# Kernel optimization log

Measured on AMD Instinct MI355X. Metric: run time of the kernel, lower is better.

## Reference

```python
import jax, jax.numpy as jnp
import numpy as np

B = 8; N_MELS = 128; T_LEN = 1024; PH = 16; PW = 16
D = 768          # embed_dim
DEPTH = 12
N = 16           # d_state
K = 4            # d_conv (mamba default)
E = 2 * D        # d_inner (expand=2)
R = 48           # dt_rank = ceil(D/16)
NC = 10
LP = (N_MELS // PH) * (T_LEN // PW)   # 512 patch tokens
MID = LP // 2                          # middle cls token position


def layer_norm(x, w, b, eps=1e-5):
    m = x.mean(-1, keepdims=True)
    v = ((x - m) ** 2).mean(-1, keepdims=True)
    return (x - m) * jax.lax.rsqrt(v + eps) * w + b


def dw_conv(x, w, b):
    # x: (B,L,E), w: (E,K) -> causal depthwise conv1d + SiLU (mamba conv branch)
    xt = jnp.transpose(x, (0, 2, 1))
    y = jax.lax.conv_general_dilated(xt, w[:, None, :], (1,), [(K - 1, 0)],
                                     feature_group_count=E,
                                     dimension_numbers=('NCH', 'OIH', 'NCH'))
    return jax.nn.silu(jnp.transpose(y + b[None, :, None], (0, 2, 1)))


def ssm(u, z, xw, dtw, dtb, A_log, Dp):
    # selective scan: u,z (B,L,E); xw (R+2N,E); dtw (E,R); A_log,Dp (E,N)/(E,)
    dbc = jnp.einsum('ble,re->blr', u, xw)
    dt, Bm, Cm = dbc[..., :R], dbc[..., R:R + N], dbc[..., R + N:]
    delta = jax.nn.softplus(jnp.einsum('blr,er->ble', dt, dtw) + dtb)
    A = -jnp.exp(A_log)  # (E,N)

    def step(h, inp):
        d_t, B_t, C_t, u_t = inp  # (B,E),(B,N),(B,N),(B,E)
        h = h * jnp.exp(d_t[:, :, None] * A) + (d_t * u_t)[:, :, None] * B_t[:, None, :]
        return h, jnp.einsum('ben,bn->be', h, C_t)

    h0 = jnp.zeros((u.shape[0], E, N), u.dtype)
    xs = (jnp.transpose(delta, (1, 0, 2)), jnp.transpose(Bm, (1, 0, 2)),
          jnp.transpose(Cm, (1, 0, 2)), jnp.transpose(u, (1, 0, 2)))
    _, ys = jax.lax.scan(step, h0, xs)
    y = jnp.transpose(ys, (1, 0, 2)) + u * Dp
    return y * jax.nn.silu(z)


def setup_inputs() -> dict:
    key = jax.random.key(0)
    kit = iter(jax.random.split(key, 64))
    def nrm(shape, s=0.02):
        return jax.random.normal(next(kit), shape, jnp.float32) * s
    inp = {}
    inp['x'] = jax.random.normal(next(kit), (B, 1, N_MELS, T_LEN), jnp.float32)
    inp['patch_w'] = nrm((D, 1, PH, PW))
    inp['patch_b'] = jnp.zeros((D,), jnp.float32)
    inp['cls_token'] = nrm((1, 1, D))
    inp['norm_w'] = jnp.ones((DEPTH, D), jnp.float32)
    inp['norm_b'] = jnp.zeros((DEPTH, D), jnp.float32)
    inp['in_proj_w'] = nrm((DEPTH, 2 * E, D))
    for s in ('f', 'b'):
        inp['conv_w_' + s] = nrm((DEPTH, E, K), 0.1)
        inp['conv_b_' + s] = jnp.zeros((DEPTH, E), jnp.float32)
        inp['x_proj_w_' + s] = nrm((DEPTH, R + 2 * N, E))
        inp['dt_proj_w_' + s] = nrm((DEPTH, E, R), 0.1)
        dt = jnp.exp(jax.random.uniform(next(kit), (DEPTH, E), jnp.float32)
                     * (np.log(0.1) - np.log(1e-3)) + np.log(1e-3))
        inp['dt_proj_b_' + s] = jnp.log(jnp.expm1(dt))  # inverse softplus init
        inp['A_log_' + s] = jnp.broadcast_to(
            jnp.log(jnp.arange(1, N + 1, dtype=jnp.float32)), (DEPTH, E, N)) + jnp.zeros((DEPTH, E, N), jnp.float32)
        inp['D_' + s] = jnp.ones((DEPTH, E), jnp.float32)
    inp['out_proj_w'] = nrm((DEPTH, D, E))
    inp['fnorm_w'] = jnp.ones((D,), jnp.float32)
    inp['fnorm_b'] = jnp.zeros((D,), jnp.float32)
    inp['head_norm_w'] = jnp.ones((D,), jnp.float32)
    inp['head_norm_b'] = jnp.zeros((D,), jnp.float32)
    inp['head_w'] = nrm((NC, D))
    inp['head_b'] = jnp.zeros((NC,), jnp.float32)
    return inp


def reference(x, patch_w, patch_b, cls_token, norm_w, norm_b, in_proj_w,
              conv_w_f, conv_b_f, conv_w_b, conv_b_b,
              x_proj_w_f, x_proj_w_b, dt_proj_w_f, dt_proj_b_f,
              dt_proj_w_b, dt_proj_b_b, A_log_f, A_log_b, D_f, D_b,
              out_proj_w, fnorm_w, fnorm_b, head_norm_w, head_norm_b,
              head_w, head_b):
    # patch embed (Conv2d, stride = patch)
    t = jax.lax.conv_general_dilated(x, patch_w, (PH, PW), 'VALID',
                                     dimension_numbers=('NCHW', 'OIHW', 'NCHW'))
    t = t + patch_b[None, :, None, None]
    b = t.shape[0]
    tok = jnp.transpose(t.reshape(b, D, -1), (0, 2, 1))  # (B, LP, D)
    cls = jnp.broadcast_to(cls_token, (b, 1, D))
    h = jnp.concatenate([tok[:, :MID], cls, tok[:, MID:]], axis=1)  # middle cls token
    for i in range(DEPTH):
        hn = layer_norm(h, norm_w[i], norm_b[i])
        xz = jnp.einsum('bld,ed->ble', hn, in_proj_w[i])
        xm, z = xz[..., :E], xz[..., E:]
        # forward direction
        xf = dw_conv(xm, conv_w_f[i], conv_b_f[i])
        yf = ssm(xf, z, x_proj_w_f[i], dt_proj_w_f[i], dt_proj_b_f[i], A_log_f[i], D_f[i])
        # backward direction (bimamba v2): scan over flipped sequence
        xr, zr = xm[:, ::-1], z[:, ::-1]
        xb = dw_conv(xr, conv_w_b[i], conv_b_b[i])
        yb = ssm(xb, zr, x_proj_w_b[i], dt_proj_w_b[i], dt_proj_b_b[i], A_log_b[i], D_b[i])[:, ::-1]
        h = h + jnp.einsum('ble,de->bld', yf + yb, out_proj_w[i])
    h = layer_norm(h, fnorm_w, fnorm_b)
    feat = h[:, MID]  # middle cls token feature
    feat = layer_norm(feat, head_norm_w, head_norm_b)
    return jnp.einsum('bd,cd->bc', feat, head_w) + head_b
```

## Files before the change

### kernel.cpp

```cpp
#include <hip/hip_runtime.h>
#include <cstddef>
#include <cstdint>

#define NB     8
#define L_SEQ  513
#define DMODEL 768
#define EDIM   1536
#define XZDIM  3072
#define NSTATE 16
#define DBCW   80
#define RDIM   48
#define ROWS   (NB*L_SEQ)
#define RE     ((size_t)ROWS*EDIM)
#define KSPLIT_DBC 8

typedef unsigned short u16;
typedef __bf16 bf16x8 __attribute__((ext_vector_type(8)));
typedef float  f32x4  __attribute__((ext_vector_type(4)));

__device__ __forceinline__ u16 f2b(float f) {
  uint32_t x = __float_as_uint(f);
  uint32_t r = x + 0x7fffu + ((x >> 16) & 1u);
  return (u16)(r >> 16);
}

__device__ __forceinline__ void glds16(const void* g, void* l) {
  __builtin_amdgcn_global_load_lds(
      (const __attribute__((address_space(1))) uint32_t*)g,
      (__attribute__((address_space(3))) uint32_t*)l, 16, 0, 0);
}

__global__ __launch_bounds__(256) void f2b_k(const float* __restrict__ in,
                                             u16* __restrict__ out, int n)
{
  int i = (blockIdx.x*256 + threadIdx.x) * 4;
  if (i >= n) return;
  float4 v = *reinterpret_cast<const float4*>(in + i);
  ushort4 o;
  o.x = f2b(v.x); o.y = f2b(v.y); o.z = f2b(v.z); o.w = f2b(v.w);
  *reinterpret_cast<ushort4*>(out + i) = o;
}

__global__ __launch_bounds__(256) void f2b2_k(const float* __restrict__ a,
                                              const float* __restrict__ b,
                                              u16* __restrict__ oa,
                                              u16* __restrict__ ob,
                                              int n1, int n2)
{
  int i = (blockIdx.x*256 + threadIdx.x) * 4;
  if (i < n1) {
    float4 v = *reinterpret_cast<const float4*>(a + i);
    ushort4 o; o.x=f2b(v.x); o.y=f2b(v.y); o.z=f2b(v.z); o.w=f2b(v.w);
    *reinterpret_cast<ushort4*>(oa + i) = o;
  } else {
    int j = i - n1;
    if (j < n2) {
      float4 v = *reinterpret_cast<const float4*>(b + j);
      ushort4 o; o.x=f2b(v.x); o.y=f2b(v.y); o.z=f2b(v.z); o.w=f2b(v.w);
      *reinterpret_cast<ushort4*>(ob + j) = o;
    }
  }
}

__global__ __launch_bounds__(256) void cvt_dtw_k(const float* __restrict__ in,
                                                 u16* __restrict__ out, int nrows)
{
  int idx = blockIdx.x*256 + threadIdx.x;
  if (idx >= nrows*16) return;
  int row = idx >> 4, c4 = (idx & 15) * 4;
  ushort4 o; o.x = o.y = o.z = o.w = 0;
  if (c4 < RDIM) {
    float4 v = *reinterpret_cast<const float4*>(in + (size_t)row*RDIM + c4);
    o.x = f2b(v.x); o.y = f2b(v.y); o.z = f2b(v.z); o.w = f2b(v.w);
  }
  *reinterpret_cast<ushort4*>(out + (size_t)row*64 + c4) = o;
}

__global__ __launch_bounds__(256) void im2col_k(const float* __restrict__ x,
                                                u16* __restrict__ P)
{
  int idx = blockIdx.x*256 + threadIdx.x;
  int col4 = (idx & 63) * 4;
  int r = idx >> 6;
  int b = r >> 9, p = r & 511;
  int ph = p >> 6, pcol = p & 63;
  int i = col4 >> 4, j = col4 & 15;
  const float* src = x + (size_t)b*131072 + (size_t)(ph*16 + i)*1024 + pcol*16 + j;
  float4 v = *reinterpret_cast<const float4*>(src);
  ushort4 o;
  o.x = f2b(v.x); o.y = f2b(v.y); o.z = f2b(v.z); o.w = f2b(v.w);
  *reinterpret_cast<ushort4*>(P + (size_t)r*256 + col4) = o;
}

__global__ __launch_bounds__(256) void insert_k(const float* __restrict__ tokf,
                                                const float* __restrict__ cls,
                                                float* __restrict__ h)
{
  int idx = blockIdx.x*256 + threadIdx.x;
  if (idx >= ROWS*192) return;
  int d4 = (idx % 192) * 4;
  int row = idx / 192;
  int b = row / L_SEQ, l = row - b*L_SEQ;
  float4 v;
  if (l == 256) v = *reinterpret_cast<const float4*>(cls + d4);
  else {
    int p = (l < 256) ? l : l - 1;
    v = *reinterpret_cast<const float4*>(tokf + ((size_t)(b*512 + p))*DMODEL + d4);
  }
  *reinterpret_cast<float4*>(h + (size_t)row*DMODEL + d4) = v;
}

__device__ __forceinline__ void wave_reduce2(float& s, float& ss) {
  #pragma unroll
  for (int o = 32; o; o >>= 1) { s += __shfl_down(s, o); ss += __shfl_down(ss, o); }
}

__global__ __launch_bounds__(256) void layernorm_k(
    const float* __restrict__ x, const float* __restrict__ w,
    const float* __restrict__ b, u16* __restrict__ y)
{
  int row = blockIdx.x;
  const float* xr = x + (size_t)row*DMODEL;
  u16*         yr = y + (size_t)row*DMODEL;
  int t = threadIdx.x;
  float v0 = xr[t], v1 = xr[t+256], v2 = xr[t+512];
  float s = v0+v1+v2, ss = v0*v0 + v1*v1 + v2*v2;
  wave_reduce2(s, ss);
  __shared__ float sm[8];
  if ((t & 63) == 0) { sm[t>>6] = s; sm[4 + (t>>6)] = ss; }
  __syncthreads();
  s  = sm[0]+sm[1]+sm[2]+sm[3];
  ss = sm[4]+sm[5]+sm[6]+sm[7];
  float mean = s * (1.f/768.f);
  float var  = ss * (1.f/768.f) - mean*mean;
  float rstd = rsqrtf(var + 1e-5f);
  yr[t]     = f2b((v0-mean)*rstd*w[t]     + b[t]);
  yr[t+256] = f2b((v1-mean)*rstd*w[t+256] + b[t+256]);
  yr[t+512] = f2b((v2-mean)*rstd*w[t+512] + b[t+512]);
}

__global__ __launch_bounds__(256) void gemm_bf16_k(
    const u16* __restrict__ A, int lda,
    const u16* __restrict__ W, int ldw,
    float* __restrict__ C, int ldc, int M, int Ncols, int K,
    const float* __restrict__ bias, int epilogue,
    int zsplit, size_t bsA, size_t bsW, size_t bsC, size_t bsBias)
{
  __shared__ __align__(16) u16 Asl[2][4096];
  __shared__ __align__(16) u16 Wsl[2][4096];
  const int tid = threadIdx.x;
  const int bm = blockIdx.y << 7, bn = blockIdx.x << 7;
  const int wv = tid >> 6, ln = tid & 63;
  const int wr = (wv >> 1) << 6, wc = (wv & 1) << 6;

  int kb = 0, ke = K;
  {
    int zb = (int)blockIdx.z;
    int dir = zb / zsplit, kslab = zb - dir*zsplit;
    A += (size_t)dir * bsA;
    W += (size_t)dir * bsW;
    C += (size_t)dir * bsC;
    if (bias) bias += (size_t)dir * bsBias;
    if (zsplit > 1) {
      int ksl = K / zsplit;
      kb = kslab * ksl; ke = kb + ksl;
      C += (size_t)kslab * (size_t)M * (size_t)ldc;
    }
  }

  const int q0 = (ln >> 4) * 8;
  const int r0 = wv*16 + (ln & 15);
  const int r1 = (wv+4)*16 + (ln & 15);

  int ar0 = bm + r0; if (ar0 >= M) ar0 = M-1;
  int ar1 = bm + r1; if (ar1 >= M) ar1 = M-1;
  int nr0 = bn + r0; if (nr0 >= Ncols) nr0 = Ncols-1;
  int nr1 = bn + r1; if (nr1 >= Ncols) nr1 = Ncols-1;
  const u16* A0 = A + (size_t)ar0*lda + q0;
  const u16* A1 = A + (size_t)ar1*lda + q0;
  const u16* W0 = W + (size_t)nr0*ldw + q0;
  const u16* W1 = W + (size_t)nr1*ldw + q0;

  auto STAGE = [&](int buf, int k0) {
    char* ab = (char*)&Asl[buf][0];
    char* wb = (char*)&Wsl[buf][0];
    glds16(A0 + k0, ab + wv*1024);
    glds16(A1 + k0, ab + 4096 + wv*1024);
    glds16(W0 + k0, wb + wv*1024);
    glds16(W1 + k0, wb + 4096 + wv*1024);
  };

  f32x4 acc[4][4];
  #pragma unroll
  for (int m = 0; m < 4; ++m)
    #pragma unroll
    for (int n = 0; n < 4; ++n) acc[m][n] = (f32x4){0.f,0.f,0.f,0.f};

  const int niter = (ke - kb) >> 5;
  STAGE(0, kb);
  for (int it = 0; it < niter; ++it) {
    const int p = it & 1;
    if (it + 1 < niter) {
      STAGE(p ^ 1, kb + (it + 1) * 32);
      asm volatile("s_waitcnt vmcnt(4)" ::: "memory");
    } else {
      asm volatile("s_waitcnt vmcnt(0)" ::: "memory");
    }
    __builtin_amdgcn_s_barrier();
    bf16x8 fa[4], fb[4];
    #pragma unroll
    for (int m = 0; m < 4; ++m)
      fa[m] = *reinterpret_cast<const bf16x8*>(&Asl[p][((wr>>4)+m)*512 + ln*8]);
    #pragma unroll
    for (int n = 0; n < 4; ++n)
      fb[n] = *reinterpret_cast<const bf16x8*>(&Wsl[p][((wc>>4)+n)*512 + ln*8]);
    #pragma unroll
    for (int m = 0; m < 4; ++m)
      #pragma unroll
      for (int n = 0; n < 4; ++n)
        acc[m][n] = __builtin_amdgcn_mfma_f32_16x16x32_bf16(fa[m], fb[n], acc[m][n], 0, 0, 0);
    __builtin_amdgcn_s_barrier();
  }

  const int crow0 = bm + wr + ((ln >> 4) << 2);
  const int ccol0 = bn + wc + (ln & 15);
  #pragma unroll
  for (int m = 0; m < 4; ++m) {
    #pragma unroll
    for (int q = 0; q < 4; ++q) {
      int row = crow0 + m*16 + q;
      if (row >= M) continue;
      float* Cr = C + (size_t)row*ldc;
      #pragma unroll
      for (int n = 0; n < 4; ++n) {
        int col = ccol0 + n*16;
        if (col >= Ncols) continue;
        float v = acc[m][n][q];
        if (epilogue == 1) v += Cr[col];
        else if (epilogue == 2) {
          v += bias[col];
          v = fmaxf(v, 0.f) + log1pf(__expf(-fabsf(v)));
        } else if (epilogue == 3) v += bias[col];
        Cr[col] = v;
      }
    }
  }
}

__global__ void reduce_split2_k(const float* __restrict__ part,
                                float* __restrict__ dbc2, u16* __restrict__ dt48,
                                int nsplit)
{
  int i = blockIdx.x * 256 + threadIdx.x;
  if (i >= 2*ROWS*DBCW) return;
  int dir = i / (ROWS*DBCW);
  int j   = i - dir*(ROWS*DBCW);
  const float* p = part + (size_t)dir*nsplit*(ROWS*DBCW);
  float s = 0.f;
  for (int z = 0; z < nsplit; ++z) s += p[(size_t)z*(ROWS*DBCW) + j];
  dbc2[i] = s;
  int row = j / DBCW, col = j - row*DBCW;
  if (col < RDIM)    dt48[(size_t)dir*ROWS*64 + (size_t)row*64 + col] = f2b(s);
  else if (col < 64) dt48[(size_t)dir*ROWS*64 + (size_t)row*64 + col] = 0;
}

__global__ __launch_bounds__(256) void dwconv_silu_k(
    const float* __restrict__ xz,
    const float* __restrict__ w_f, const float* __restrict__ w_b,
    const float* __restrict__ b_f, const float* __restrict__ b_b,
    u16* __restrict__ outb2)
{
  const int dir = blockIdx.y;
  const float* w    = dir ? w_b : w_f;
  const float* bias = dir ? b_b : b_f;
  u16* outb = outb2 + (size_t)dir*RE;
  int idx = blockIdx.x * 256 + threadIdx.x;
  int r = idx / (EDIM/4);
  int e4 = (idx - r*(EDIM/4)) * 4;
  int b = r / L_SEQ, t = r - b*L_SEQ;
  float4 acc = *reinterpret_cast<const float4*>(&bias[e4]);
  float4 wq0 = *reinterpret_cast<const float4*>(&w[(size_t)(e4+0)*4]);
  float4 wq1 = *reinterpret_cast<const float4*>(&w[(size_t)(e4+1)*4]);
  float4 wq2 = *reinterpret_cast<const float4*>(&w[(size_t)(e4+2)*4]);
  float4 wq3 = *reinterpret_cast<const float4*>(&w[(size_t)(e4+3)*4]);
  #pragma unroll
  for (int k = 0; k < 4; ++k) {
    int tt = t - 3 + k;
    if (tt >= 0) {
      int phys = dir ? (L_SEQ-1 - tt) : tt;
      float4 xv = *reinterpret_cast<const float4*>(
          &xz[((size_t)b*L_SEQ + phys)*XZDIM + e4]);
      float w0 = (k==0)?wq0.x:(k==1)?wq0.y:(k==2)?wq0.z:wq0.w;
      float w1 = (k==0)?wq1.x:(k==1)?wq1.y:(k==2)?wq1.z:wq1.w;
      float w2 = (k==0)?wq2.x:(k==1)?wq2.y:(k==2)?wq2.z:wq2.w;
      float w3 = (k==0)?wq3.x:(k==1)?wq3.y:(k==2)?wq3.z:wq3.w;
      acc.x = fmaf(xv.x, w0, acc.x);
      acc.y = fmaf(xv.y, w1, acc.y);
      acc.z = fmaf(xv.z, w2, acc.z);
      acc.w = fmaf(xv.w, w3, acc.w);
    }
  }
  float4 sv;
  sv.x = acc.x / (1.f + __expf(-acc.x));
  sv.y = acc.y / (1.f + __expf(-acc.y));
  sv.z = acc.z / (1.f + __expf(-acc.z));
  sv.w = acc.w / (1.f + __expf(-acc.w));
  ushort4 ob;
  ob.x = f2b(sv.x); ob.y = f2b(sv.y); ob.z = f2b(sv.z); ob.w = f2b(sv.w);
  *reinterpret_cast<ushort4*>(&outb[(size_t)r*EDIM + e4]) = ob;
}

__device__ __forceinline__ float dpp_reduce16(float v) {
  v += __int_as_float(__builtin_amdgcn_update_dpp(0, __float_as_int(v), 0x111, 0xf, 0xf, true));
  v += __int_as_float(__builtin_amdgcn_update_dpp(0, __float_as_int(v), 0x112, 0xf, 0xf, true));
  v += __int_as_float(__builtin_amdgcn_update_dpp(0, __float_as_int(v), 0x114, 0xf, 0xf, true));
  v += __int_as_float(__builtin_amdgcn_update_dpp(0, __float_as_int(v), 0x118, 0xf, 0xf, true));
  return v;
}

#define TC 32
#define NCH ((L_SEQ + TC - 1) / TC)

__global__ __launch_bounds__(256) void ssm_scan_k(
    const float* __restrict__ delta2, const u16* __restrict__ ub2,
    const float* __restrict__ dbc2,
    const float* __restrict__ Alf, const float* __restrict__ Alb,
    const float* __restrict__ Dpf, const float* __restrict__ Dpb,
    const float* __restrict__ xz,  u16* __restrict__ yhalf)
{
  __shared__ __align__(16) float dd[2][TC][16];
  __shared__ __align__(16) float us[2][TC][16];
  __shared__ __align__(16) float Bs[2][16][TC+4];
  __shared__ __align__(16) float Cs[2][16][TC+4];
  __shared__ __align__(16) float yb[TC][16];

  const int dir = blockIdx.z;
  const float* delta = delta2 + (size_t)dir*RE;
  const u16*   ub    = ub2    + (size_t)dir*RE;
  const float* dbc   = dbc2   + (size_t)dir*ROWS*DBCW;
  const float* A_log = dir ? Alb : Alf;
  const float* Dp    = dir ? Dpb : Dpf;
  u16* yh = yhalf + (size_t)dir*RE;

  const int tid = threadIdx.x;
  const int g = tid >> 4, n = tid & 15;
  const int b = blockIdx.y;
  const int e0 = blockIdx.x * 16;
  const int e = e0 + g;
  const size_t rb = (size_t)b * L_SEQ;

  const float a  = -__expf(A_log[(size_t)e*NSTATE + n]);
  const float dp = Dp[e];

  const int ss_ = tid >> 3;
  const int c2  = (tid & 7) * 2;
  const int j4  = (tid & 7) * 4;

  float2 dv = make_float2(0,0);
  uint32_t uv = 0;
  float4 bcv = make_float4(0,0,0,0);

  auto LOAD = [&](int c) {
    int Tn = min(TC, L_SEQ - c*TC);
    if (ss_ < Tn) {
      size_t r = rb + c*TC + ss_;
      dv  = *reinterpret_cast<const float2*>(&delta[r*EDIM + e0 + c2]);
      uv  = *reinterpret_cast<const uint32_t*>(&ub[r*EDIM + e0 + c2]);
      bcv = *reinterpret_cast<const float4*>(&dbc[r*DBCW + RDIM + j4]);
    }
  };
  auto STORE = [&](int p, int c) {
    int Tn = min(TC, L_SEQ - c*TC);
    if (ss_ < Tn) {
      dd[p][ss_][c2] = dv.x; dd[p][ss_][c2+1] = dv.y;
      us[p][ss_][c2]   = __uint_as_float((uv & 0xffffu) << 16);
      us[p][ss_][c2+1] = __uint_as_float(uv & 0xffff0000u);
      if (j4 < 16) {
        Bs[p][j4  ][ss_] = bcv.x; Bs[p][j4+1][ss_] = bcv.y;
        Bs[p][j4+2][ss_] = bcv.z; Bs[p][j4+3][ss_] = bcv.w;
      } else {
        Cs[p][j4-16][ss_] = bcv.x; Cs[p][j4-15][ss_] = bcv.y;
        Cs[p][j4-14][ss_] = bcv.z; Cs[p][j4-13][ss_] = bcv.w;
      }
    }
  };

  float hst = 0.f;
  LOAD(0);
  STORE(0, 0);
  __syncthreads();

  int p = 0;
  for (int c = 0; c < NCH; ++c) {
    const int t0 = c * TC;
    const int T  = min(TC, L_SEQ - t0);
    if (c + 1 < NCH) LOAD(c + 1);

    int s = 0;
    for (; s + 3 < T; s += 4) {
      float4 Bv = *reinterpret_cast<const float4*>(&Bs[p][n][s]);
      float4 Cv = *reinterpret_cast<const float4*>(&Cs[p][n][s]);
      #pragma unroll
      for (int i = 0; i < 4; ++i) {
        float Bt = (i==0)?Bv.x:(i==1)?Bv.y:(i==2)?Bv.z:Bv.w;
        float Ct = (i==0)?Cv.x:(i==1)?Cv.y:(i==2)?Cv.z:Cv.w;
        float d  = dd[p][s+i][g];
        float uu = us[p][s+i][g];
        hst = fmaf(hst, __expf(d*a), d*uu*Bt);
        float yp = dpp_reduce16(hst * Ct);
        if (n == 15) yb[s+i][g] = yp + uu*dp;
      }
    }
    for (; s < T; ++s) {
      float Bt = Bs[p][n][s], Ct = Cs[p][n][s];
      float d  = dd[p][s][g];
      float uu = us[p][s][g];
      hst = fmaf(hst, __expf(d*a), d*uu*Bt);
      float yp = dpp_reduce16(hst * Ct);
      if (n == 15) yb[s][g] = yp + uu*dp;
    }
    __syncthreads();

    if (ss_ < T) {
      int t = t0 + ss_;
      int phys = dir ? (L_SEQ-1 - t) : t;
      size_t pr = rb + phys;
      float2 yv = *reinterpret_cast<const float2*>(&yb[ss_][c2]);
      float2 zv = *reinterpret_cast<const float2*>(&xz[pr*XZDIM + EDIM + e0 + c2]);
      ushort2 o;
      o.x = f2b(yv.x * (zv.x / (1.f + __expf(-zv.x))));
      o.y = f2b(yv.y * (zv.y / (1.f + __expf(-zv.y))));
      *reinterpret_cast<ushort2*>(&yh[pr*EDIM + e0 + c2]) = o;
    }
    if (c + 1 < NCH) STORE(p ^ 1, c + 1);
    __syncthreads();
    p ^= 1;
  }
}

__global__ __launch_bounds__(256) void add_ybf_k(const u16* __restrict__ yhalf,
                                                 u16* __restrict__ ybf)
{
  size_t i = ((size_t)blockIdx.x*256 + threadIdx.x) * 8;
  uint4 a = *reinterpret_cast<const uint4*>(yhalf + i);
  uint4 b = *reinterpret_cast<const uint4*>(yhalf + RE + i);
  uint32_t av[4] = {a.x, a.y, a.z, a.w};
  uint32_t bv[4] = {b.x, b.y, b.z, b.w};
  uint32_t ov[4];
  #pragma unroll
  for (int q = 0; q < 4; ++q) {
    float lo = __uint_as_float((av[q] & 0xffffu) << 16) +
               __uint_as_float((bv[q] & 0xffffu) << 16);
    float hi = __uint_as_float(av[q] & 0xffff0000u) +
               __uint_as_float(bv[q] & 0xffff0000u);
    ov[q] = (uint32_t)f2b(lo) | ((uint32_t)f2b(hi) << 16);
  }
  uint4 o = {ov[0], ov[1], ov[2], ov[3]};
  *reinterpret_cast<uint4*>(ybf + i) = o;
}

__global__ __launch_bounds__(256) void head_k(
    const float* __restrict__ h,
    const float* __restrict__ fnw, const float* __restrict__ fnb,
    const float* __restrict__ hnw, const float* __restrict__ hnb,
    const float* __restrict__ hw,  const float* __restrict__ hb,
    float* __restrict__ out)
{
  int b = blockIdx.x, t = threadIdx.x;
  const float* xr = h + ((size_t)b*L_SEQ + 256)*DMODEL;
  __shared__ float feat[DMODEL];
  __shared__ float sm[8];
  float v0 = xr[t], v1 = xr[t+256], v2 = xr[t+512];
  float s = v0+v1+v2, ss = v0*v0+v1*v1+v2*v2;
  wave_reduce2(s, ss);
  if ((t & 63) == 0) { sm[t>>6] = s; sm[4+(t>>6)] = ss; }
  __syncthreads();
  s = sm[0]+sm[1]+sm[2]+sm[3]; ss = sm[4]+sm[5]+sm[6]+sm[7];
  float mean = s*(1.f/768.f), var = ss*(1.f/768.f) - mean*mean;
  float rstd = rsqrtf(var + 1e-5f);
  float f0 = (v0-mean)*rstd*fnw[t]     + fnb[t];
  float f1 = (v1-mean)*rstd*fnw[t+256] + fnb[t+256];
  float f2 = (v2-mean)*rstd*fnw[t+512] + fnb[t+512];
  s = f0+f1+f2; ss = f0*f0+f1*f1+f2*f2;
  wave_reduce2(s, ss);
  __syncthreads();
  if ((t & 63) == 0) { sm[t>>6] = s; sm[4+(t>>6)] = ss; }
  __syncthreads();
  s = sm[0]+sm[1]+sm[2]+sm[3]; ss = sm[4]+sm[5]+sm[6]+sm[7];
  mean = s*(1.f/768.f); var = ss*(1.f/768.f) - mean*mean;
  rstd = rsqrtf(var + 1e-5f);
  feat[t]     = (f0-mean)*rstd*hnw[t]     + hnb[t];
  feat[t+256] = (f1-mean)*rstd*hnw[t+256] + hnb[t+256];
  feat[t+512] = (f2-mean)*rstd*hnw[t+512] + hnb[t+512];
  __syncthreads();
  for (int c = 0; c < 10; ++c) {
    float d = 0.f;
    for (int i = t; i < DMODEL; i += 256) d = fmaf(feat[i], hw[(size_t)c*DMODEL + i], d);
    #pragma unroll
    for (int o = 32; o; o >>= 1) d += __shfl_down(d, o);
    __syncthreads();
    if ((t & 63) == 0) sm[t>>6] = d;
    __syncthreads();
    if (t == 0) out[b*10 + c] = sm[0]+sm[1]+sm[2]+sm[3] + hb[c];
  }
}

extern "C" void kernel_launch(void* const* d_in, const int* in_sizes, int n_in,
                              void* d_out, int out_size, void* d_ws, size_t ws_size,
                              hipStream_t stream)
{
  (void)in_sizes; (void)n_in; (void)out_size; (void)ws_size;
  const float* x           = (const float*)d_in[0];
  const float* patch_w     = (const float*)d_in[1];
  const float* patch_b     = (const float*)d_in[2];
  const float* cls_tok     = (const float*)d_in[3];
  const float* norm_w      = (const float*)d_in[4];
  const float* norm_b      = (const float*)d_in[5];
  const float* in_proj_w   = (const float*)d_in[6];
  const float* conv_w_f    = (const float*)d_in[7];
  const float* conv_b_f    = (const float*)d_in[8];
  const float* x_proj_w_f  = (const float*)d_in[9];
  const float* dt_proj_w_f = (const float*)d_in[10];
  const float* dt_proj_b_f = (const float*)d_in[11];
  const float* A_log_f     = (const float*)d_in[12];
  const float* D_f         = (const float*)d_in[13];
  const float* conv_w_b    = (const float*)d_in[14];
  const float* conv_b_b    = (const float*)d_in[15];
  const float* x_proj_w_b  = (const float*)d_in[16];
  const float* dt_proj_w_b = (const float*)d_in[17];
  const float* dt_proj_b_b = (const float*)d_in[18];
  const float* A_log_b     = (const float*)d_in[19];
  const float* D_b         = (const float*)d_in[20];
  const float* out_proj_w  = (const float*)d_in[21];
  const float* fnorm_w     = (const float*)d_in[22];
  const float* fnorm_b     = (const float*)d_in[23];
  const float* head_norm_w = (const float*)d_in[24];
  const float* head_norm_b = (const float*)d_in[25];
  const float* head_w      = (const float*)d_in[26];
  const float* head_b      = (const float*)d_in[27];
  float* out = (float*)d_out;

  float* ws = (float*)d_ws;
  float* h      = ws;        ws += (size_t)ROWS*DMODEL;
  u16*   hn     = (u16*)ws;  ws += RE/2;
  u16*   ybf    = hn;
  float* xz     = ws;        ws += (size_t)ROWS*XZDIM;
  u16*   ubufb2 = (u16*)ws;  ws += RE;
  float* dbc2   = ws;        ws += (size_t)2*ROWS*DBCW;
  u16*   dt48b2 = (u16*)ws;  ws += (size_t)2*ROWS*64/2;
  float* delta2 = ws;        ws += 2*RE;
  u16*   yhalf  = (u16*)ws;  ws += RE;
  u16*   wbf_a  = (u16*)ws;  ws += (size_t)XZDIM*DMODEL/2;
  u16*   wbf_b  = (u16*)ws;  ws += (size_t)DMODEL*EDIM/2;
  u16*   pwbf   = (u16*)ws;  ws += (size_t)DMODEL*256/2;
  u16*   xwbf   = (u16*)ws;  ws += (size_t)2*12*DBCW*EDIM/2;
  u16*   dtwbf  = (u16*)ws;  ws += (size_t)2*12*EDIM*64/2;
  float* dtb2   = ws;        ws += (size_t)2*12*EDIM;
  float* dbcp   = delta2;
  u16*   Pim    = ubufb2;
  float* tokf   = delta2;

  f2b_k<<<(DMODEL*256)/1024, 256, 0, stream>>>(patch_w, pwbf, DMODEL*256);
  f2b_k<<<(12*DBCW*EDIM)/1024, 256, 0, stream>>>(x_proj_w_f, xwbf, 12*DBCW*EDIM);
  f2b_k<<<(12*DBCW*EDIM)/1024, 256, 0, stream>>>(x_proj_w_b, xwbf + (size_t)12*DBCW*EDIM, 12*DBCW*EDIM);
  cvt_dtw_k<<<(12*EDIM*16)/256, 256, 0, stream>>>(dt_proj_w_f, dtwbf, 12*EDIM);
  cvt_dtw_k<<<(12*EDIM*16)/256, 256, 0, stream>>>(dt_proj_w_b, dtwbf + (size_t)12*EDIM*64, 12*EDIM);
  hipMemcpyAsync(dtb2,           dt_proj_b_f, (size_t)12*EDIM*4, hipMemcpyDeviceToDevice, stream);
  hipMemcpyAsync(dtb2 + 12*EDIM, dt_proj_b_b, (size_t)12*EDIM*4, hipMemcpyDeviceToDevice, stream);

  im2col_k<<<(4096*64)/256, 256, 0, stream>>>(x, Pim);
  {
    dim3 g(DMODEL/128, 4096/128);
    gemm_bf16_k<<<g, 256, 0, stream>>>(Pim, 256, pwbf, 256, tokf, DMODEL,
                                       4096, DMODEL, 256, patch_b, 3,
                                       1, 0, 0, 0, 0);
  }
  insert_k<<<(ROWS*192 + 255)/256, 256, 0, stream>>>(tokf, cls_tok, h);

  const int MT = (ROWS + 127)/128;

  for (int i = 0; i < 12; ++i) {
    f2b2_k<<<(XZDIM*DMODEL + DMODEL*EDIM)/1024, 256, 0, stream>>>(
        in_proj_w + (size_t)i*XZDIM*DMODEL, out_proj_w + (size_t)i*DMODEL*EDIM,
        wbf_a, wbf_b, XZDIM*DMODEL, DMODEL*EDIM);
    layernorm_k<<<ROWS, 256, 0, stream>>>(h, norm_w + (size_t)i*DMODEL,
                                          norm_b + (size_t)i*DMODEL, hn);
    {
      dim3 g(XZDIM/128, MT);
      gemm_bf16_k<<<g, 256, 0, stream>>>(hn, DMODEL, wbf_a, DMODEL,
                                         xz, XZDIM, ROWS, XZDIM, DMODEL, nullptr, 0,
                                         1, 0, 0, 0, 0);
    }
    {
      dim3 g((ROWS*EDIM/4)/256, 2);
      dwconv_silu_k<<<g, 256, 0, stream>>>(xz,
          conv_w_f + (size_t)i*EDIM*4, conv_w_b + (size_t)i*EDIM*4,
          conv_b_f + (size_t)i*EDIM,   conv_b_b + (size_t)i*EDIM, ubufb2);
    }
    {
      dim3 g(1, MT, 2*KSPLIT_DBC);
      gemm_bf16_k<<<g, 256, 0, stream>>>(ubufb2, EDIM,
          xwbf + (size_t)i*DBCW*EDIM, EDIM,
          dbcp, DBCW, ROWS, DBCW, EDIM, nullptr, 0,
          KSPLIT_DBC, RE, (size_t)12*DBCW*EDIM, (size_t)KSPLIT_DBC*ROWS*DBCW, 0);
      reduce_split2_k<<<(2*ROWS*DBCW + 255)/256, 256, 0, stream>>>(
          dbcp, dbc2, dt48b2, KSPLIT_DBC);
    }
    {
      dim3 g(EDIM/128, MT, 2);
      gemm_bf16_k<<<g, 256, 0, stream>>>(dt48b2, 64,
          dtwbf + (size_t)i*EDIM*64, 64,
          delta2, EDIM, ROWS, EDIM, 64, dtb2 + (size_t)i*EDIM, 2,
          1, (size_t)ROWS*64, (size_t)12*EDIM*64, RE, (size_t)12*EDIM);
    }
    {
      dim3 g(EDIM/16, NB, 2);
      ssm_scan_k<<<g, 256, 0, stream>>>(delta2, ubufb2, dbc2,
          A_log_f + (size_t)i*EDIM*NSTATE, A_log_b + (size_t)i*EDIM*NSTATE,
          D_f + (size_t)i*EDIM, D_b + (size_t)i*EDIM, xz, yhalf);
    }
    add_ybf_k<<<(int)(RE/8/256), 256, 0, stream>>>(yhalf, ybf);
    {
      dim3 g(DMODEL/128, MT);
      gemm_bf16_k<<<g, 256, 0, stream>>>(ybf, EDIM, wbf_b, EDIM,
                                         h, DMODEL, ROWS, DMODEL, EDIM, nullptr, 1,
                                         1, 0, 0, 0, 0);
    }
  }

  head_k<<<NB, 256, 0, stream>>>(h, fnorm_w, fnorm_b, head_norm_w, head_norm_b,
                                 head_w, head_b, out);
}
```

Baseline: 4.619 ms.

## Fuse bidirectional output sum into out-proj GEMM and narrow scan intermediates to bf16

The out_proj weight is duplicated along K, and the scan writes forward and backward outputs interleaved per row. The out-projection GEMM then runs with K=3072 and sums both directions itself, so the separate add kernel goes away. The in-proj GEMM now writes xm as fp32 and z as bf16 into separate buffers. Delta is stored in bf16 instead of fp32, and the scan's per-state reduction changes from a 16-lane DPP reduce to quad sums plus an LDS partial-sum buffer, with exp2f replacing expf. This cuts memory traffic and one launch in exchange for doubling the out-proj GEMM's K and lowering the precision of delta and z.

Result: slower. 5.299 ms (+14.7%).

```diff
diff --git a/kernel.cpp b/kernel.cpp
--- a/kernel.cpp
+++ b/kernel.cpp
@@ -23,6 +23,8 @@
   uint32_t r = x + 0x7fffu + ((x >> 16) & 1u);
   return (u16)(r >> 16);
 }
+__device__ __forceinline__ float b2flo(uint32_t w){ return __uint_as_float(w << 16); }
+__device__ __forceinline__ float b2fhi(uint32_t w){ return __uint_as_float(w & 0xffff0000u); }
 
 __device__ __forceinline__ void glds16(const void* g, void* l) {
   __builtin_amdgcn_global_load_lds(
@@ -57,7 +59,10 @@
     if (j < n2) {
       float4 v = *reinterpret_cast<const float4*>(b + j);
       ushort4 o; o.x=f2b(v.x); o.y=f2b(v.y); o.z=f2b(v.z); o.w=f2b(v.w);
-      *reinterpret_cast<ushort4*>(ob + j) = o;
+      int row = j / EDIM, col = j - row*EDIM;
+      u16* dst = ob + (size_t)row*XZDIM + col;
+      *reinterpret_cast<ushort4*>(dst)        = o;
+      *reinterpret_cast<ushort4*>(dst + EDIM) = o;
     }
   }
 }
@@ -142,7 +147,8 @@
 __global__ __launch_bounds__(256) void gemm_bf16_k(
     const u16* __restrict__ A, int lda,
     const u16* __restrict__ W, int ldw,
-    float* __restrict__ C, int ldc, int M, int Ncols, int K,
+    float* __restrict__ C, u16* __restrict__ Cb,
+    int ldc, int M, int Ncols, int K,
     const float* __restrict__ bias, int epilogue,
     int zsplit, size_t bsA, size_t bsW, size_t bsC, size_t bsBias)
 {
@@ -159,7 +165,8 @@
     int dir = zb / zsplit, kslab = zb - dir*zsplit;
     A += (size_t)dir * bsA;
     W += (size_t)dir * bsW;
-    C += (size_t)dir * bsC;
+    if (C)  C  += (size_t)dir * bsC;
+    if (Cb) Cb += (size_t)dir * bsC;
     if (bias) bias += (size_t)dir * bsBias;
     if (zsplit > 1) {
       int ksl = K / zsplit;
@@ -230,18 +237,25 @@
     for (int q = 0; q < 4; ++q) {
       int row = crow0 + m*16 + q;
       if (row >= M) continue;
-      float* Cr = C + (size_t)row*ldc;
       #pragma unroll
       for (int n = 0; n < 4; ++n) {
         int col = ccol0 + n*16;
         if (col >= Ncols) continue;
         float v = acc[m][n][q];
-        if (epilogue == 1) v += Cr[col];
-        else if (epilogue == 2) {
+        if (epilogue == 0) {
+          C[(size_t)row*ldc + col] = v;
+        } else if (epilogue == 1) {
+          C[(size_t)row*ldc + col] += v;
+        } else if (epilogue == 2) {
           v += bias[col];
           v = fmaxf(v, 0.f) + log1pf(__expf(-fabsf(v)));
-        } else if (epilogue == 3) v += bias[col];
-        Cr[col] = v;
+          Cb[(size_t)row*ldc + col] = f2b(v);
+        } else if (epilogue == 3) {
+          C[(size_t)row*ldc + col] = v + bias[col];
+        } else {
+          if (col < EDIM) C[(size_t)row*EDIM + col] = v;
+          else            Cb[(size_t)row*EDIM + (col - EDIM)] = f2b(v);
+        }
       }
     }
   }
@@ -265,7 +279,7 @@
 }
 
 __global__ __launch_bounds__(256) void dwconv_silu_k(
-    const float* __restrict__ xz,
+    const float* __restrict__ xm,
     const float* __restrict__ w_f, const float* __restrict__ w_b,
     const float* __restrict__ b_f, const float* __restrict__ b_b,
     u16* __restrict__ outb2)
@@ -289,7 +303,7 @@
     if (tt >= 0) {
       int phys = dir ? (L_SEQ-1 - tt) : tt;
       float4 xv = *reinterpret_cast<const float4*>(
-          &xz[((size_t)b*L_SEQ + phys)*XZDIM + e4]);
+          &xm[((size_t)b*L_SEQ + phys)*EDIM + e4]);
       float w0 = (k==0)?wq0.x:(k==1)?wq0.y:(k==2)?wq0.z:wq0.w;
       float w1 = (k==0)?wq1.x:(k==1)?wq1.y:(k==2)?wq1.z:wq1.w;
       float w2 = (k==0)?wq2.x:(k==1)?wq2.y:(k==2)?wq2.z:wq2.w;
@@ -310,11 +324,9 @@
   *reinterpret_cast<ushort4*>(&outb[(size_t)r*EDIM + e4]) = ob;
 }
 
-__device__ __forceinline__ float dpp_reduce16(float v) {
-  v += __int_as_float(__builtin_amdgcn_update_dpp(0, __float_as_int(v), 0x111, 0xf, 0xf, true));
-  v += __int_as_float(__builtin_amdgcn_update_dpp(0, __float_as_int(v), 0x112, 0xf, 0xf, true));
-  v += __int_as_float(__builtin_amdgcn_update_dpp(0, __float_as_int(v), 0x114, 0xf, 0xf, true));
-  v += __int_as_float(__builtin_amdgcn_update_dpp(0, __float_as_int(v), 0x118, 0xf, 0xf, true));
+__device__ __forceinline__ float quad_sum(float v) {
+  v += __int_as_float(__builtin_amdgcn_update_dpp(0, __float_as_int(v), 0xB1, 0xf, 0xf, true));
+  v += __int_as_float(__builtin_amdgcn_update_dpp(0, __float_as_int(v), 0x4E, 0xf, 0xf, true));
   return v;
 }
 
@@ -322,59 +334,57 @@
 #define NCH ((L_SEQ + TC - 1) / TC)
 
 __global__ __launch_bounds__(256) void ssm_scan_k(
-    const float* __restrict__ delta2, const u16* __restrict__ ub2,
+    const u16* __restrict__ deltab2, const u16* __restrict__ ub2,
     const float* __restrict__ dbc2,
     const float* __restrict__ Alf, const float* __restrict__ Alb,
     const float* __restrict__ Dpf, const float* __restrict__ Dpb,
-    const float* __restrict__ xz,  u16* __restrict__ yhalf)
+    const u16* __restrict__ zb,  u16* __restrict__ yhalf)
 {
   __shared__ __align__(16) float dd[2][TC][16];
   __shared__ __align__(16) float us[2][TC][16];
   __shared__ __align__(16) float Bs[2][16][TC+4];
   __shared__ __align__(16) float Cs[2][16][TC+4];
-  __shared__ __align__(16) float yb[TC][16];
+  __shared__ __align__(16) float hc[TC][16][4];
 
   const int dir = blockIdx.z;
-  const float* delta = delta2 + (size_t)dir*RE;
-  const u16*   ub    = ub2    + (size_t)dir*RE;
-  const float* dbc   = dbc2   + (size_t)dir*ROWS*DBCW;
+  const u16*   db  = deltab2 + (size_t)dir*RE;
+  const u16*   ub  = ub2     + (size_t)dir*RE;
+  const float* dbc = dbc2    + (size_t)dir*ROWS*DBCW;
   const float* A_log = dir ? Alb : Alf;
   const float* Dp    = dir ? Dpb : Dpf;
-  u16* yh = yhalf + (size_t)dir*RE;
 
   const int tid = threadIdx.x;
   const int g = tid >> 4, n = tid & 15;
   const int b = blockIdx.y;
   const int e0 = blockIdx.x * 16;
-  const int e = e0 + g;
   const size_t rb = (size_t)b * L_SEQ;
 
-  const float a  = -__expf(A_log[(size_t)e*NSTATE + n]);
-  const float dp = Dp[e];
+  const float a2 = -__expf(A_log[(size_t)(e0+g)*NSTATE + n]) * 1.44269504f;
+  const bool wlane = (n & 3) == 0;
+  const int  qn = n >> 2;
 
   const int ss_ = tid >> 3;
   const int c2  = (tid & 7) * 2;
   const int j4  = (tid & 7) * 4;
-
-  float2 dv = make_float2(0,0);
-  uint32_t uv = 0;
+  const float dp0 = Dp[e0 + c2], dp1 = Dp[e0 + c2 + 1];
+
+  uint32_t dvb = 0, uvb = 0;
   float4 bcv = make_float4(0,0,0,0);
 
   auto LOAD = [&](int c) {
     int Tn = min(TC, L_SEQ - c*TC);
     if (ss_ < Tn) {
       size_t r = rb + c*TC + ss_;
-      dv  = *reinterpret_cast<const float2*>(&delta[r*EDIM + e0 + c2]);
-      uv  = *reinterpret_cast<const uint32_t*>(&ub[r*EDIM + e0 + c2]);
+      dvb = *reinterpret_cast<const uint32_t*>(&db[r*EDIM + e0 + c2]);
+      uvb = *reinterpret_cast<const uint32_t*>(&ub[r*EDIM + e0 + c2]);
       bcv = *reinterpret_cast<const float4*>(&dbc[r*DBCW + RDIM + j4]);
     }
   };
   auto STORE = [&](int p, int c) {
     int Tn = min(TC, L_SEQ - c*TC);
     if (ss_ < Tn) {
-      dd[p][ss_][c2] = dv.x; dd[p][ss_][c2+1] = dv.y;
-      us[p][ss_][c2]   = __uint_as_float((uv & 0xffffu) << 16);
-      us[p][ss_][c2+1] = __uint_as_float(uv & 0xffff0000u);
+      dd[p][ss_][c2] = b2flo(dvb); dd[p][ss_][c2+1] = b2fhi(dvb);
+      us[p][ss_][c2] = b2flo(uvb); us[p][ss_][c2+1] = b2fhi(uvb);
       if (j4 < 16) {
         Bs[p][j4  ][ss_] = bcv.x; Bs[p][j4+1][ss_] = bcv.y;
         Bs[p][j4+2][ss_] = bcv.z; Bs[p][j4+3][ss_] = bcv.w;
@@ -406,18 +416,18 @@
         float Ct = (i==0)?Cv.x:(i==1)?Cv.y:(i==2)?Cv.z:Cv.w;
         float d  = dd[p][s+i][g];
         float uu = us[p][s+i][g];
-        hst = fmaf(hst, __expf(d*a), d*uu*Bt);
-        float yp = dpp_reduce16(hst * Ct);
-        if (n == 15) yb[s+i][g] = yp + uu*dp;
+        hst = fmaf(hst, exp2f(d * a2), (d * uu) * Bt);
+        float v = quad_sum(hst * Ct);
+        if (wlane) hc[s+i][g][qn] = v;
       }
     }
     for (; s < T; ++s) {
       float Bt = Bs[p][n][s], Ct = Cs[p][n][s];
       float d  = dd[p][s][g];
       float uu = us[p][s][g];
-      hst = fmaf(hst, __expf(d*a), d*uu*Bt);
-      float yp = dpp_reduce16(hst * Ct);
-      if (n == 15) yb[s][g] = yp + uu*dp;
+      hst = fmaf(hst, exp2f(d * a2), (d * uu) * Bt);
+      float v = quad_sum(hst * Ct);
+      if (wlane) hc[s][g][qn] = v;
     }
     __syncthreads();
 
@@ -425,38 +435,23 @@
       int t = t0 + ss_;
       int phys = dir ? (L_SEQ-1 - t) : t;
       size_t pr = rb + phys;
-      float2 yv = *reinterpret_cast<const float2*>(&yb[ss_][c2]);
-      float2 zv = *reinterpret_cast<const float2*>(&xz[pr*XZDIM + EDIM + e0 + c2]);
-      ushort2 o;
-      o.x = f2b(yv.x * (zv.x / (1.f + __expf(-zv.x))));
-      o.y = f2b(yv.y * (zv.y / (1.f + __expf(-zv.y))));
-      *reinterpret_cast<ushort2*>(&yh[pr*EDIM + e0 + c2]) = o;
+      float4 p0 = *reinterpret_cast<const float4*>(&hc[ss_][c2][0]);
+      float4 p1 = *reinterpret_cast<const float4*>(&hc[ss_][c2+1][0]);
+      float y0 = (p0.x + p0.y) + (p0.z + p0.w);
+      float y1 = (p1.x + p1.y) + (p1.z + p1.w);
+      y0 = fmaf(us[p][ss_][c2],   dp0, y0);
+      y1 = fmaf(us[p][ss_][c2+1], dp1, y1);
+      uint32_t zw = *reinterpret_cast<const uint32_t*>(&zb[pr*EDIM + e0 + c2]);
+      float z0 = b2flo(zw), z1 = b2fhi(zw);
+      y0 *= z0 / (1.f + __expf(-z0));
+      y1 *= z1 / (1.f + __expf(-z1));
+      ushort2 o; o.x = f2b(y0); o.y = f2b(y1);
+      *reinterpret_cast<ushort2*>(&yhalf[((size_t)pr*2 + dir)*EDIM + e0 + c2]) = o;
     }
     if (c + 1 < NCH) STORE(p ^ 1, c + 1);
     __syncthreads();
     p ^= 1;
   }
-}
-
-__global__ __launch_bounds__(256) void add_ybf_k(const u16* __restrict__ yhalf,
-                                                 u16* __restrict__ ybf)
-{
-  size_t i = ((size_t)blockIdx.x*256 + threadIdx.x) * 8;
-  uint4 a = *reinterpret_cast<const uint4*>(yhalf + i);
-  uint4 b = *reinterpret_cast<const uint4*>(yhalf + RE + i);
-  uint32_t av[4] = {a.x, a.y, a.z, a.w};
-  uint32_t bv[4] = {b.x, b.y, b.z, b.w};
-  uint32_t ov[4];
-  #pragma unroll
-  for (int q = 0; q < 4; ++q) {
-    float lo = __uint_as_float((av[q] & 0xffffu) << 16) +
-               __uint_as_float((bv[q] & 0xffffu) << 16);
-    float hi = __uint_as_float(av[q] & 0xffff0000u) +
-               __uint_as_float(bv[q] & 0xffff0000u);
-    ov[q] = (uint32_t)f2b(lo) | ((uint32_t)f2b(hi) << 16);
-  }
-  uint4 o = {ov[0], ov[1], ov[2], ov[3]};
-  *reinterpret_cast<uint4*>(ybf + i) = o;
 }
 
 __global__ __launch_bounds__(256) void head_k(
@@ -541,24 +536,24 @@
   float* out = (float*)d_out;
 
   float* ws = (float*)d_ws;
-  float* h      = ws;        ws += (size_t)ROWS*DMODEL;
-  u16*   hn     = (u16*)ws;  ws += RE/2;
-  u16*   ybf    = hn;
-  float* xz     = ws;        ws += (size_t)ROWS*XZDIM;
-  u16*   ubufb2 = (u16*)ws;  ws += RE;
-  float* dbc2   = ws;        ws += (size_t)2*ROWS*DBCW;
-  u16*   dt48b2 = (u16*)ws;  ws += (size_t)2*ROWS*64/2;
-  float* delta2 = ws;        ws += 2*RE;
-  u16*   yhalf  = (u16*)ws;  ws += RE;
-  u16*   wbf_a  = (u16*)ws;  ws += (size_t)XZDIM*DMODEL/2;
-  u16*   wbf_b  = (u16*)ws;  ws += (size_t)DMODEL*EDIM/2;
-  u16*   pwbf   = (u16*)ws;  ws += (size_t)DMODEL*256/2;
-  u16*   xwbf   = (u16*)ws;  ws += (size_t)2*12*DBCW*EDIM/2;
-  u16*   dtwbf  = (u16*)ws;  ws += (size_t)2*12*EDIM*64/2;
-  float* dtb2   = ws;        ws += (size_t)2*12*EDIM;
-  float* dbcp   = delta2;
-  u16*   Pim    = ubufb2;
-  float* tokf   = delta2;
+  float* h       = ws;        ws += (size_t)ROWS*DMODEL;
+  u16*   hn      = (u16*)ws;  ws += (size_t)ROWS*DMODEL/2;
+  float* xmf     = ws;        ws += RE;
+  u16*   zb16    = (u16*)ws;  ws += RE/2;
+  u16*   ubufb2  = (u16*)ws;  ws += RE;
+  float* dbc2    = ws;        ws += (size_t)2*ROWS*DBCW;
+  u16*   dt48b2  = (u16*)ws;  ws += (size_t)2*ROWS*64/2;
+  u16*   deltab2 = (u16*)ws;  ws += RE;
+  u16*   yhalf2  = (u16*)ws;  ws += RE;
+  u16*   wbf_a   = (u16*)ws;  ws += (size_t)XZDIM*DMODEL/2;
+  u16*   wbdup   = (u16*)ws;  ws += (size_t)DMODEL*XZDIM/2;
+  u16*   pwbf    = (u16*)ws;  ws += (size_t)DMODEL*256/2;
+  u16*   xwbf    = (u16*)ws;  ws += (size_t)2*12*DBCW*EDIM/2;
+  u16*   dtwbf   = (u16*)ws;  ws += (size_t)2*12*EDIM*64/2;
+  float* dtb2    = ws;        ws += (size_t)2*12*EDIM;
+  float* dbcp    = (float*)deltab2;
+  u16*   Pim     = ubufb2;
+  float* tokf    = (float*)deltab2;
 
   f2b_k<<<(DMODEL*256)/1024, 256, 0, stream>>>(patch_w, pwbf, DMODEL*256);
   f2b_k<<<(12*DBCW*EDIM)/1024, 256, 0, stream>>>(x_proj_w_f, xwbf, 12*DBCW*EDIM);
@@ -571,8 +566,8 @@
   im2col_k<<<(4096*64)/256, 256, 0, stream>>>(x, Pim);
   {
     dim3 g(DMODEL/128, 4096/128);
-    gemm_bf16_k<<<g, 256, 0, stream>>>(Pim, 256, pwbf, 256, tokf, DMODEL,
-                                       4096, DMODEL, 256, patch_b, 3,
+    gemm_bf16_k<<<g, 256, 0, stream>>>(Pim, 256, pwbf, 256, tokf, nullptr,
+                                       DMODEL, 4096, DMODEL, 256, patch_b, 3,
                                        1, 0, 0, 0, 0);
   }
   insert_k<<<(ROWS*192 + 255)/256, 256, 0, stream>>>(tokf, cls_tok, h);
@@ -582,18 +577,18 @@
   for (int i = 0; i < 12; ++i) {
     f2b2_k<<<(XZDIM*DMODEL + DMODEL*EDIM)/1024, 256, 0, stream>>>(
         in_proj_w + (size_t)i*XZDIM*DMODEL, out_proj_w + (size_t)i*DMODEL*EDIM,
-        wbf_a, wbf_b, XZDIM*DMODEL, DMODEL*EDIM);
+        wbf_a, wbdup, XZDIM*DMODEL, DMODEL*EDIM);
     layernorm_k<<<ROWS, 256, 0, stream>>>(h, norm_w + (size_t)i*DMODEL,
                                           norm_b + (size_t)i*DMODEL, hn);
     {
       dim3 g(XZDIM/128, MT);
       gemm_bf16_k<<<g, 256, 0, stream>>>(hn, DMODEL, wbf_a, DMODEL,
-                                         xz, XZDIM, ROWS, XZDIM, DMODEL, nullptr, 0,
-                                         1, 0, 0, 0, 0);
+                                         xmf, zb16, EDIM, ROWS, XZDIM, DMODEL,
+                                         nullptr, 4, 1, 0, 0, 0, 0);
     }
     {
       dim3 g((ROWS*EDIM/4)/256, 2);
-      dwconv_silu_k<<<g, 256, 0, stream>>>(xz,
+      dwconv_silu_k<<<g, 256, 0, stream>>>(xmf,
           conv_w_f + (size_t)i*EDIM*4, conv_w_b + (size_t)i*EDIM*4,
           conv_b_f + (size_t)i*EDIM,   conv_b_b + (size_t)i*EDIM, ubufb2);
     }
@@ -601,7 +596,7 @@
       dim3 g(1, MT, 2*KSPLIT_DBC);
       gemm_bf16_k<<<g, 256, 0, stream>>>(ubufb2, EDIM,
           xwbf + (size_t)i*DBCW*EDIM, EDIM,
-          dbcp, DBCW, ROWS, DBCW, EDIM, nullptr, 0,
+          dbcp, nullptr, DBCW, ROWS, DBCW, EDIM, nullptr, 0,
           KSPLIT_DBC, RE, (size_t)12*DBCW*EDIM, (size_t)KSPLIT_DBC*ROWS*DBCW, 0);
       reduce_split2_k<<<(2*ROWS*DBCW + 255)/256, 256, 0, stream>>>(
           dbcp, dbc2, dt48b2, KSPLIT_DBC);
@@ -610,21 +605,20 @@
       dim3 g(EDIM/128, MT, 2);
       gemm_bf16_k<<<g, 256, 0, stream>>>(dt48b2, 64,
           dtwbf + (size_t)i*EDIM*64, 64,
-          delta2, EDIM, ROWS, EDIM, 64, dtb2 + (size_t)i*EDIM, 2,
+          nullptr, deltab2, EDIM, ROWS, EDIM, 64, dtb2 + (size_t)i*EDIM, 2,
           1, (size_t)ROWS*64, (size_t)12*EDIM*64, RE, (size_t)12*EDIM);
     }
     {
       dim3 g(EDIM/16, NB, 2);
-      ssm_scan_k<<<g, 256, 0, stream>>>(delta2, ubufb2, dbc2,
+      ssm_scan_k<<<g, 256, 0, stream>>>(deltab2, ubufb2, dbc2,
           A_log_f + (size_t)i*EDIM*NSTATE, A_log_b + (size_t)i*EDIM*NSTATE,
-          D_f + (size_t)i*EDIM, D_b + (size_t)i*EDIM, xz, yhalf);
-    }
-    add_ybf_k<<<(int)(RE/8/256), 256, 0, stream>>>(yhalf, ybf);
+          D_f + (size_t)i*EDIM, D_b + (size_t)i*EDIM, zb16, yhalf2);
+    }
     {
       dim3 g(DMODEL/128, MT);
-      gemm_bf16_k<<<g, 256, 0, stream>>>(ybf, EDIM, wbf_b, EDIM,
-                                         h, DMODEL, ROWS, DMODEL, EDIM, nullptr, 1,
-                                         1, 0, 0, 0, 0);
+      gemm_bf16_k<<<g, 256, 0, stream>>>(yhalf2, XZDIM, wbdup, XZDIM,
+                                         h, nullptr, DMODEL, ROWS, DMODEL, XZDIM,
+                                         nullptr, 1, 1, 0, 0, 0, 0);
     }
   }
 
```

## Split-K out_proj GEMM into partials with reduce-add, and interleave delta/u in LDS

Applied to the files above, without the earlier changes.

The out_proj GEMM (K=1536, N=768) now runs with a 4-way K split. Each split writes fp32 partials into the delta2 scratch buffer, and a new vectorized kernel sums the four partials and adds them into the residual h. The aim is to raise block count and occupancy for a GEMM that only has 6 column tiles. The cost is extra global traffic, about 4x ROWS*DMODEL floats written and read again, plus one more launch. The scan kernel also interleaves delta and u in one shared array, so each step reads both with a single float2 LDS load instead of two.

New measurement: 4.438 ms. 1.04x faster.

```diff
diff --git a/kernel.cpp b/kernel.cpp
--- a/kernel.cpp
+++ b/kernel.cpp
@@ -262,6 +262,24 @@
   int row = j / DBCW, col = j - row*DBCW;
   if (col < RDIM)    dt48[(size_t)dir*ROWS*64 + (size_t)row*64 + col] = f2b(s);
   else if (col < 64) dt48[(size_t)dir*ROWS*64 + (size_t)row*64 + col] = 0;
+}
+
+__global__ __launch_bounds__(256) void reduce4_addh_k(const float* __restrict__ part,
+                                                      float* __restrict__ h)
+{
+  size_t i = ((size_t)blockIdx.x*256 + threadIdx.x) * 4;
+  if (i >= (size_t)ROWS*DMODEL) return;
+  const size_t S = (size_t)ROWS*DMODEL;
+  float4 s0 = *reinterpret_cast<const float4*>(part + i);
+  float4 s1 = *reinterpret_cast<const float4*>(part + S + i);
+  float4 s2 = *reinterpret_cast<const float4*>(part + 2*S + i);
+  float4 s3 = *reinterpret_cast<const float4*>(part + 3*S + i);
+  float4 hv = *reinterpret_cast<const float4*>(h + i);
+  hv.x += (s0.x + s1.x) + (s2.x + s3.x);
+  hv.y += (s0.y + s1.y) + (s2.y + s3.y);
+  hv.z += (s0.z + s1.z) + (s2.z + s3.z);
+  hv.w += (s0.w + s1.w) + (s2.w + s3.w);
+  *reinterpret_cast<float4*>(h + i) = hv;
 }
 
 __global__ __launch_bounds__(256) void dwconv_silu_k(
@@ -328,8 +346,7 @@
     const float* __restrict__ Dpf, const float* __restrict__ Dpb,
     const float* __restrict__ xz,  u16* __restrict__ yhalf)
 {
-  __shared__ __align__(16) float dd[2][TC][16];
-  __shared__ __align__(16) float us[2][TC][16];
+  __shared__ __align__(16) float du[2][TC][16][2];
   __shared__ __align__(16) float Bs[2][16][TC+4];
   __shared__ __align__(16) float Cs[2][16][TC+4];
   __shared__ __align__(16) float yb[TC][16];
@@ -372,9 +389,10 @@
   auto STORE = [&](int p, int c) {
     int Tn = min(TC, L_SEQ - c*TC);
     if (ss_ < Tn) {
-      dd[p][ss_][c2] = dv.x; dd[p][ss_][c2+1] = dv.y;
-      us[p][ss_][c2]   = __uint_as_float((uv & 0xffffu) << 16);
-      us[p][ss_][c2+1] = __uint_as_float(uv & 0xffff0000u);
+      float2 w0 = make_float2(dv.x, __uint_as_float((uv & 0xffffu) << 16));
+      float2 w1 = make_float2(dv.y, __uint_as_float(uv & 0xffff0000u));
+      *reinterpret_cast<float2*>(&du[p][ss_][c2][0])   = w0;
+      *reinterpret_cast<float2*>(&du[p][ss_][c2+1][0]) = w1;
       if (j4 < 16) {
         Bs[p][j4  ][ss_] = bcv.x; Bs[p][j4+1][ss_] = bcv.y;
         Bs[p][j4+2][ss_] = bcv.z; Bs[p][j4+3][ss_] = bcv.w;
@@ -404,8 +422,9 @@
       for (int i = 0; i < 4; ++i) {
         float Bt = (i==0)?Bv.x:(i==1)?Bv.y:(i==2)?Bv.z:Bv.w;
         float Ct = (i==0)?Cv.x:(i==1)?Cv.y:(i==2)?Cv.z:Cv.w;
-        float d  = dd[p][s+i][g];
-        float uu = us[p][s+i][g];
+        float2 duv = *reinterpret_cast<const float2*>(&du[p][s+i][g][0]);
+        float d  = duv.x;
+        float uu = duv.y;
         hst = fmaf(hst, __expf(d*a), d*uu*Bt);
         float yp = dpp_reduce16(hst * Ct);
         if (n == 15) yb[s+i][g] = yp + uu*dp;
@@ -413,8 +432,9 @@
     }
     for (; s < T; ++s) {
       float Bt = Bs[p][n][s], Ct = Cs[p][n][s];
-      float d  = dd[p][s][g];
-      float uu = us[p][s][g];
+      float2 duv = *reinterpret_cast<const float2*>(&du[p][s][g][0]);
+      float d  = duv.x;
+      float uu = duv.y;
       hst = fmaf(hst, __expf(d*a), d*uu*Bt);
       float yp = dpp_reduce16(hst * Ct);
       if (n == 15) yb[s][g] = yp + uu*dp;
@@ -557,6 +577,7 @@
   u16*   dtwbf  = (u16*)ws;  ws += (size_t)2*12*EDIM*64/2;
   float* dtb2   = ws;        ws += (size_t)2*12*EDIM;
   float* dbcp   = delta2;
+  float* opart  = delta2;
   u16*   Pim    = ubufb2;
   float* tokf   = delta2;
 
@@ -621,10 +642,11 @@
     }
     add_ybf_k<<<(int)(RE/8/256), 256, 0, stream>>>(yhalf, ybf);
     {
-      dim3 g(DMODEL/128, MT);
+      dim3 g(DMODEL/128, MT, 4);
       gemm_bf16_k<<<g, 256, 0, stream>>>(ybf, EDIM, wbf_b, EDIM,
-                                         h, DMODEL, ROWS, DMODEL, EDIM, nullptr, 1,
-                                         1, 0, 0, 0, 0);
+                                         opart, DMODEL, ROWS, DMODEL, EDIM, nullptr, 0,
+                                         4, 0, 0, 0, 0);
+      reduce4_addh_k<<<(int)(((size_t)ROWS*DMODEL/4 + 255)/256), 256, 0, stream>>>(opart, h);
     }
   }
 
```
